# Kernel optimization log

Hardware: AMD Instinct MI355X
Metric: run time of the kernel (lower is better)

Reference implementation:

```python
import jax, jax.numpy as jnp
import numpy as np

N, E = 20000, 320000          # nodes, edges (avg in-degree ~16)
F_IN, EMB, T, OUT = 40, 40, 5, 2
F_T = EMB // T                # per-tower output width = 8
EPS_STD, EPS_GN = 1e-5, 1e-5


def _lin_init(k, fan_in, fan_out, extra=()):
    return jax.random.normal(k, (*extra, fan_in, fan_out), jnp.float32) / np.sqrt(fan_in)


def setup_inputs() -> dict:
    key = jax.random.key(0)
    ks = jax.random.split(key, 8)
    # deg histogram in init: all 20000 nodes with degree 16 -> avg_deg['log'] = log(16+1)
    return dict(
        x=jax.random.normal(ks[0], (N, F_IN), jnp.float32),
        edge_index=jax.random.randint(ks[1], (2, E), 0, N),
        W_pre=_lin_init(ks[2], 2 * F_IN, F_IN, (T,)),   # per-tower pre-MLP
        b_pre=jnp.zeros((T, F_IN), jnp.float32),
        W_post=_lin_init(ks[3], 13 * F_IN, F_T, (T,)),  # (4 agg * 3 scalers + 1 residual) * F_in
        b_post=jnp.zeros((T, F_T), jnp.float32),
        W_lin=_lin_init(ks[4], T * F_T, EMB),           # PNAConv final mixing linear
        b_lin=jnp.zeros((EMB,), jnp.float32),
        gn_weight=jnp.ones((EMB,), jnp.float32),
        gn_bias=jnp.zeros((EMB,), jnp.float32),
        gn_mean_scale=jnp.ones((EMB,), jnp.float32),
        W1=_lin_init(ks[5], EMB, EMB),                  # head hidden linear
        b1=jnp.zeros((EMB,), jnp.float32),
        W2=_lin_init(ks[6], EMB, OUT),                  # head output linear
        b2=jnp.zeros((OUT,), jnp.float32),
        avg_deg_log=jnp.float32(np.log(17.0)),
    )


def _pna_conv(x, src, dst, W_pre, b_pre, W_post, b_post, W_lin, b_lin, avg_deg_log):
    xi, xj = x[dst], x[src]                              # gather: [E, F]
    h = jnp.concatenate([xi, xj], axis=-1)               # [E, 2F]
    m = jnp.einsum('ef,tfg->etg', h, W_pre) + b_pre      # per-tower messages [E, T, F]
    cnt = jax.ops.segment_sum(jnp.ones((E,), m.dtype), dst, num_segments=N)  # in-degree [N]
    denom = jnp.maximum(cnt, 1.0)[:, None, None]
    mean = jax.ops.segment_sum(m, dst, num_segments=N) / denom
    mean2 = jax.ops.segment_sum(m * m, dst, num_segments=N) / denom
    std = jnp.sqrt(jax.nn.relu(mean2 - mean * mean) + EPS_STD)
    has = (cnt > 0)[:, None, None]
    mn = jnp.where(has, jax.ops.segment_min(m, dst, num_segments=N), 0.0)
    mx = jnp.where(has, jax.ops.segment_max(m, dst, num_segments=N), 0.0)
    agg = jnp.concatenate([mean, mn, mx, std], axis=-1)  # [N, T, 4F]
    deg = jnp.maximum(cnt, 1.0)[:, None, None]
    logd = jnp.log(deg + 1.0)
    out = jnp.concatenate(
        [agg, agg * (logd / avg_deg_log), agg * (avg_deg_log / logd)], axis=-1)  # [N, T, 12F]
    out = jnp.concatenate(
        [jnp.broadcast_to(x[:, None, :], (N, T, x.shape[-1])), out], axis=-1)    # [N, T, 13F]
    out = jnp.einsum('ntf,tfg->ntg', out, W_post) + b_post                       # [N, T, F_T]
    return out.reshape(N, T * F_T) @ W_lin + b_lin


def _graph_norm(x, w, b, mean_scale):
    mean = jnp.mean(x, axis=0, keepdims=True)
    out = x - mean_scale * mean
    var = jnp.mean(out * out, axis=0, keepdims=True)
    return w * out / jnp.sqrt(var + EPS_GN) + b


def reference(x, edge_index, W_pre, b_pre, W_post, b_post, W_lin, b_lin,
              gn_weight, gn_bias, gn_mean_scale, W1, b1, W2, b2, avg_deg_log):
    src, dst = edge_index[0], edge_index[1]
    h = _pna_conv(x, src, dst, W_pre, b_pre, W_post, b_post, W_lin, b_lin, avg_deg_log)
    h = jax.nn.relu(_graph_norm(h, gn_weight, gn_bias, gn_mean_scale))
    h = jax.nn.relu(h @ W1 + b1)   # dropout_rate=None -> no dropout
    return h @ W2 + b2
```

## Files before the change

kernel.cpp:

```cpp
#include <hip/hip_runtime.h>
#include <math.h>

#define N_NODES 20000
#define N_EDGES 320000
#define F_IN 40
#define T_TOW 5
#define EMB 40
#define NPB_PRE 16
#define NBLK_MIX 313
#define NBLK_PM 313
#define ECHUNK 16
#define STRIDE 64

typedef __attribute__((ext_vector_type(8))) _Float16 half8;
typedef __attribute__((ext_vector_type(2))) _Float16 half2_t;
typedef __attribute__((ext_vector_type(4))) float f32x4;

#define WS_STATS   0
#define WS_CURSOR  320
#define WS_SSRC    80384
#define WS_MS      5200384
#define WS_MD      13200384
#define WS_AGG     21200384
#define WS_XPOST   53200384
#define WS_H0T     69200384
#define WS_PART    72400384

__global__ __launch_bounds__(256) void k_pre(const float* __restrict__ x,
                                             const float* __restrict__ W_pre,
                                             const float* __restrict__ b_pre,
                                             const float* __restrict__ W_post,
                                             const float* __restrict__ b_post,
                                             _Float16* __restrict__ mS,
                                             _Float16* __restrict__ mD,
                                             float* __restrict__ xpostT,
                                             int* __restrict__ cursor) {
  const int tid = threadIdx.x;
  const int n0 = blockIdx.x * NPB_PRE;
  if (tid < NPB_PRE) cursor[n0 + tid] = (n0 + tid) * STRIDE;
  const bool statlane = tid < 200;
  const int q = tid - 200;
  const bool xplane = (q >= 0 && q < 40);
  const int tc = statlane ? tid : 199;
  const int t = tc / 40, g = tc - t * 40;
  const int t2 = xplane ? q / 8 : 0, g2 = xplane ? q - (q / 8) * 8 : 0;
  float wA[40], wB[40];
  const float* Wt = W_pre + t * 3200;
#pragma unroll
  for (int j = 0; j < 40; ++j) {
    wA[j] = statlane ? Wt[j * 40 + g] : W_post[t2 * 4160 + j * 8 + g2];
    wB[j] = statlane ? Wt[(40 + j) * 40 + g] : 0.f;
  }
  const float bias = statlane ? b_pre[t * 40 + g] : b_post[t2 * 8 + g2];
  for (int ni = 0; ni < NPB_PRE; ++ni) {
    const int n = n0 + ni;
    const float* xr = x + n * F_IN;
    float aA = bias, aB = 0.f;
#pragma unroll
    for (int j = 0; j < 40; j += 4) {
      const float4 xv = *(const float4*)(xr + j);
      aA += xv.x * wA[j] + xv.y * wA[j + 1] + xv.z * wA[j + 2] + xv.w * wA[j + 3];
      aB += xv.x * wB[j] + xv.y * wB[j + 1] + xv.z * wB[j + 2] + xv.w * wB[j + 3];
    }
    if (statlane) {
      mD[n * 200 + tc] = (_Float16)aA;
      mS[n * 200 + tc] = (_Float16)aB;
    } else if (xplane) {
      xpostT[t2 * (N_NODES * 8) + n * 8 + g2] = aA;
    }
  }
}

__global__ __launch_bounds__(256) void k_scatter(const int* __restrict__ src,
                                                 const int* __restrict__ dst,
                                                 int* __restrict__ cursor,
                                                 int* __restrict__ ssrc) {
  int i = blockIdx.x * 256 + threadIdx.x;
  if (i < N_EDGES) {
    int d = dst[i];
    int pos = atomicAdd(&cursor[d], 1);
    ssrc[pos] = src[i];
  }
}

__global__ __launch_bounds__(256) void k_edge(const _Float16* __restrict__ mS,
                                              const _Float16* __restrict__ mD,
                                              const int* __restrict__ cursor,
                                              const int* __restrict__ ssrc,
                                              _Float16* __restrict__ aggS) {
  const int lane = threadIdx.x & 63;
  const int wv = threadIdx.x >> 6;
  const int n = blockIdx.x * 4 + wv;
  const int r0 = n * STRIDE;
  const int r1 = __builtin_amdgcn_readfirstlane(cursor[n]);
  const int cnt = r1 - r0;
  const int cpa = lane;
  const bool bact = lane < 36;
  const int cpb = bact ? 64 + lane : 99;
  const half2_t mda = ((const half2_t*)(mD + n * 200))[cpa];
  const half2_t mdb = ((const half2_t*)(mD + n * 200))[cpb];

  const _Float16 HINF = (_Float16)65504.f;
  half2_t suma = {0, 0}, ssqa = {0, 0}, sumb = {0, 0}, ssqb = {0, 0};
  half2_t mna = {HINF, HINF}, mxa = {-HINF, -HINF};
  half2_t mnb = {HINF, HINF}, mxb = {-HINF, -HINF};
  half2_t va = {0, 0}, vb = {0, 0};

  if (cnt > 0) {
    for (int p = r0; p < r1; p += ECHUNK) {
      half2_t ha[ECHUNK], hb[ECHUNK];
#pragma unroll
      for (int i = 0; i < ECHUNK; ++i) {
        const int qe = (p + i < r1) ? (p + i) : (r1 - 1);
        const int s = __builtin_amdgcn_readfirstlane(ssrc[qe]);
        const half2_t* row = (const half2_t*)(mS + s * 200);
        ha[i] = row[cpa];
        hb[i] = row[cpb];
      }
#pragma unroll
      for (int i = 0; i < ECHUNK; ++i) {
        suma += ha[i];
        ssqa += ha[i] * ha[i];
        mna = __builtin_elementwise_min(mna, ha[i]);
        mxa = __builtin_elementwise_max(mxa, ha[i]);
        sumb += hb[i];
        ssqb += hb[i] * hb[i];
        mnb = __builtin_elementwise_min(mnb, hb[i]);
        mxb = __builtin_elementwise_max(mxb, hb[i]);
      }
      va = ha[ECHUNK - 1];
      vb = hb[ECHUNK - 1];
    }
  }

  const int padded = ((cnt + ECHUNK - 1) / ECHUNK) * ECHUNK;
  const float d = (float)(padded - cnt);
  const float inv = (cnt > 0) ? 1.f / (float)cnt : 0.f;
#pragma unroll
  for (int set = 0; set < 2; ++set) {
    if (set == 1 && !bact) break;
    const int cp = set == 0 ? cpa : cpb;
    const half2_t sum2 = set == 0 ? suma : sumb;
    const half2_t ssq2 = set == 0 ? ssqa : ssqb;
    const half2_t mn2 = set == 0 ? mna : mnb;
    const half2_t mx2 = set == 0 ? mxa : mxb;
    const half2_t vl2 = set == 0 ? va : vb;
    const half2_t md2 = set == 0 ? mda : mdb;
    half2_t omean, omn, omx, osd;
#pragma unroll
    for (int j = 0; j < 2; ++j) {
      float mean, mnf, mxf, sd;
      if (cnt > 0) {
        const float vl = (float)vl2[j];
        const float sf = (float)sum2[j] - d * vl;
        const float qf = (float)ssq2[j] - d * vl * vl;
        const float msm = sf * inv;
        const float var = qf * inv - msm * msm;
        sd = sqrtf(fmaxf(var, 0.f) + 1e-5f);
        const float mdf = (float)md2[j];
        mean = mdf + msm;
        mnf = mdf + (float)mn2[j];
        mxf = mdf + (float)mx2[j];
      } else {
        mean = 0.f; mnf = 0.f; mxf = 0.f; sd = sqrtf(1e-5f);
      }
      omean[j] = (_Float16)mean;
      omn[j] = (_Float16)mnf;
      omx[j] = (_Float16)mxf;
      osd[j] = (_Float16)sd;
    }
    const int t = cp / 20, g = 2 * (cp - t * 20);
    _Float16* abase = aggS + ((size_t)t * N_NODES + n) * 160 + g;
    *(half2_t*)(abase) = omean;
    *(half2_t*)(abase + 40) = omn;
    *(half2_t*)(abase + 80) = omx;
    *(half2_t*)(abase + 120) = osd;
  }
}

__global__ __launch_bounds__(320) void k_postmix(const _Float16* __restrict__ aggT,
                                                 const int* __restrict__ cursor,
                                                 const float* __restrict__ W_post,
                                                 const float* __restrict__ avg_dl,
                                                 const float* __restrict__ xpostT,
                                                 const float* __restrict__ W_lin,
                                                 const float* __restrict__ b_lin,
                                                 float* __restrict__ h0T,
                                                 float* __restrict__ partial) {
  __shared__ float sP[64 * 41];
  const int tid = threadIdx.x;
  const int t = tid >> 6;
  const int l = tid & 63;
  const int n0 = blockIdx.x * 64;
  const int c = l & 15;
  const int kg = l >> 4;

  const float* Wt = W_post + t * 4160;
  half8 b1f[5], b2f[5];
#pragma unroll
  for (int ks = 0; ks < 5; ++ks) {
#pragma unroll
    for (int j = 0; j < 8; ++j) {
      const int k = ks * 32 + kg * 8 + j;
      const float w1v = (c < 8) ? Wt[(40 + k) * 8 + c] : Wt[(200 + k) * 8 + (c - 8)];
      const float w2v = (c < 8) ? Wt[(360 + k) * 8 + c] : 0.f;
      b1f[ks][j] = (_Float16)w1v;
      b2f[ks][j] = (_Float16)w2v;
    }
  }
  const float avg = avg_dl[0];

  for (int tile = 0; tile < 4; ++tile) {
    const int nb = n0 + tile * 16;
    int nA = nb + c;
    if (nA >= N_NODES) nA = N_NODES - 1;
    const half8* ar = (const half8*)(aggT + ((size_t)t * N_NODES + nA) * 160);
    half8 af[5];
#pragma unroll
    for (int ks = 0; ks < 5; ++ks) af[ks] = ar[ks * 4 + kg];
    f32x4 acc1 = {0.f, 0.f, 0.f, 0.f}, acc2 = {0.f, 0.f, 0.f, 0.f};
#pragma unroll
    for (int ks = 0; ks < 5; ++ks) {
      acc1 = __builtin_amdgcn_mfma_f32_16x16x32_f16(af[ks], b1f[ks], acc1, 0, 0, 0);
      acc2 = __builtin_amdgcn_mfma_f32_16x16x32_f16(af[ks], b2f[ks], acc2, 0, 0, 0);
    }
    float bp[4];
#pragma unroll
    for (int r = 0; r < 4; ++r) bp[r] = __shfl_xor(acc1[r], 8, 64);
    if (c < 8) {
#pragma unroll
      for (int r = 0; r < 4; ++r) {
        const int nn0 = nb + kg * 4 + r;
        const int nn = (nn0 < N_NODES) ? nn0 : N_NODES - 1;
        const int cnt = cursor[nn] - nn * STRIDE;
        const float ld = logf(fmaxf((float)cnt, 1.f) + 1.f);
        const float s1 = ld / avg, s2 = avg / ld;
        const float xp = xpostT[t * (N_NODES * 8) + nn * 8 + c];
        sP[(tile * 16 + kg * 4 + r) * 41 + t * 8 + c] =
            acc1[r] + s1 * bp[r] + s2 * acc2[r] + xp;
      }
    }
  }
  __syncthreads();

  const int c0 = t * 8;
  float acc[8];
#pragma unroll
  for (int j = 0; j < 8; ++j) acc[j] = b_lin[c0 + j];
  for (int k = 0; k < 40; ++k) {
    const float p = sP[l * 41 + k];
    const float* w = W_lin + k * EMB + c0;
#pragma unroll
    for (int j = 0; j < 8; ++j) acc[j] = fmaf(p, w[j], acc[j]);
  }
  const int n = n0 + l;
  const bool ok = n < N_NODES;
  if (ok) {
#pragma unroll
    for (int j = 0; j < 8; ++j) h0T[(c0 + j) * N_NODES + n] = acc[j];
  }
#pragma unroll
  for (int j = 0; j < 8; ++j) {
    float sv = ok ? acc[j] : 0.f;
    float qv = sv * sv;
#pragma unroll
    for (int m = 32; m >= 1; m >>= 1) {
      sv += __shfl_xor(sv, m, 64);
      qv += __shfl_xor(qv, m, 64);
    }
    if (l == 0) {
      partial[blockIdx.x * 80 + c0 + j] = sv;
      partial[blockIdx.x * 80 + 40 + c0 + j] = qv;
    }
  }
}

__global__ __launch_bounds__(256) void k_stats(const float* __restrict__ partial,
                                               float* __restrict__ S1,
                                               float* __restrict__ S2) {
  const int col = blockIdx.x;
  const int tid = threadIdx.x;
  __shared__ float red[4];
  float s = 0.f;
  for (int b = tid; b < NBLK_PM; b += 256) s += partial[b * 80 + col];
#pragma unroll
  for (int m = 32; m >= 1; m >>= 1) s += __shfl_xor(s, m, 64);
  if ((tid & 63) == 0) red[tid >> 6] = s;
  __syncthreads();
  if (tid == 0) {
    const float tot = (red[0] + red[1]) + (red[2] + red[3]);
    if (col < 40) S1[col] = tot;
    else S2[col - 40] = tot;
  }
}

__global__ __launch_bounds__(256) void k_head(const float* __restrict__ S1,
                                              const float* __restrict__ S2,
                                              const float* __restrict__ h0T,
                                              const float* __restrict__ gn_w,
                                              const float* __restrict__ gn_b,
                                              const float* __restrict__ gn_ms,
                                              const float* __restrict__ W1,
                                              const float* __restrict__ b1,
                                              const float* __restrict__ W2,
                                              const float* __restrict__ b2,
                                              float* __restrict__ out) {
  __shared__ float sV[64 * 41];
  __shared__ float sH[64 * 41];
  const int tid = threadIdx.x;
  const int n0 = blockIdx.x * 64;
  const float invN = 1.f / (float)N_NODES;
  for (int i = 0; i < 10; ++i) {
    const int idx = tid + i * 256;
    const int e = idx >> 6, r = idx & 63;
    const int nn0 = n0 + r;
    const int nn = (nn0 < N_NODES) ? nn0 : 0;
    const float M = S1[e] * invN;
    const float ms = gn_ms[e];
    const float var = S2[e] * invN - ms * (2.f - ms) * M * M;
    const float sc = gn_w[e] / sqrtf(var + 1e-5f);
    const float he = h0T[e * N_NODES + nn];
    sV[r * 41 + e] = fmaxf((he - ms * M) * sc + gn_b[e], 0.f);
  }
  __syncthreads();
  const int wv = tid >> 6, lane = tid & 63;
  const int c0 = wv * 10;
  float acc[10];
#pragma unroll
  for (int j = 0; j < 10; ++j) acc[j] = b1[c0 + j];
  for (int k = 0; k < 40; ++k) {
    const float p = sV[lane * 41 + k];
    const float* w = W1 + k * EMB + c0;
#pragma unroll
    for (int j = 0; j < 10; ++j) acc[j] = fmaf(p, w[j], acc[j]);
  }
#pragma unroll
  for (int j = 0; j < 10; ++j) sH[lane * 41 + c0 + j] = fmaxf(acc[j], 0.f);
  __syncthreads();
  if (tid < 64) {
    const int n = n0 + tid;
    if (n < N_NODES) {
      float o0 = b2[0], o1 = b2[1];
      const float* hr = sH + tid * 41;
#pragma unroll
      for (int k = 0; k < 40; ++k) {
        const float r = hr[k];
        o0 = fmaf(r, W2[k * 2], o0);
        o1 = fmaf(r, W2[k * 2 + 1], o1);
      }
      out[n * 2] = o0;
      out[n * 2 + 1] = o1;
    }
  }
}

extern "C" void kernel_launch(void* const* d_in, const int* in_sizes, int n_in,
                              void* d_out, int out_size, void* d_ws, size_t ws_size,
                              hipStream_t stream) {
  const float* x      = (const float*)d_in[0];
  const int*   ei     = (const int*)d_in[1];
  const float* W_pre  = (const float*)d_in[2];
  const float* b_pre  = (const float*)d_in[3];
  const float* W_post = (const float*)d_in[4];
  const float* b_post = (const float*)d_in[5];
  const float* W_lin  = (const float*)d_in[6];
  const float* b_lin  = (const float*)d_in[7];
  const float* gn_w   = (const float*)d_in[8];
  const float* gn_b   = (const float*)d_in[9];
  const float* gn_ms  = (const float*)d_in[10];
  const float* W1     = (const float*)d_in[11];
  const float* b1     = (const float*)d_in[12];
  const float* W2     = (const float*)d_in[13];
  const float* b2     = (const float*)d_in[14];
  const float* avg_dl = (const float*)d_in[15];
  float* out = (float*)d_out;

  char* ws = (char*)d_ws;
  float* S1   = (float*)(ws + WS_STATS);
  float* S2   = S1 + 40;
  int* cursor = (int*)(ws + WS_CURSOR);
  int* ssrc   = (int*)(ws + WS_SSRC);
  _Float16* mS   = (_Float16*)(ws + WS_MS);
  _Float16* mD   = (_Float16*)(ws + WS_MD);
  _Float16* aggS = (_Float16*)(ws + WS_AGG);
  float* xpostT  = (float*)(ws + WS_XPOST);
  float* h0T     = (float*)(ws + WS_H0T);
  float* part    = (float*)(ws + WS_PART);
  const int* e_src = ei;
  const int* e_dst = ei + N_EDGES;

  k_pre<<<N_NODES / NPB_PRE, 256, 0, stream>>>(x, W_pre, b_pre, W_post, b_post,
                                               mS, mD, xpostT, cursor);
  k_scatter<<<(N_EDGES + 255) / 256, 256, 0, stream>>>(e_src, e_dst, cursor, ssrc);
  k_edge<<<N_NODES / 4, 256, 0, stream>>>(mS, mD, cursor, ssrc, aggS);
  k_postmix<<<NBLK_PM, 320, 0, stream>>>(aggS, cursor, W_post, avg_dl,
                                         xpostT, W_lin, b_lin, h0T, part);
  k_stats<<<80, 256, 0, stream>>>(part, S1, S2);
  k_head<<<NBLK_MIX, 256, 0, stream>>>(S1, S2, h0T, gn_w, gn_b, gn_ms,
                                       W1, b1, W2, b2, out);
}
```

Before: 191.7 us.

## Fuse postmix, stats and head kernels via a grid-wide atomic barrier

```diff
diff --git a/kernel.cpp b/kernel.cpp
--- a/kernel.cpp
+++ b/kernel.cpp
@@ -7,7 +7,6 @@
 #define T_TOW 5
 #define EMB 40
 #define NPB_PRE 16
-#define NBLK_MIX 313
 #define NBLK_PM 313
 #define ECHUNK 16
 #define STRIDE 64
@@ -16,7 +15,7 @@
 typedef __attribute__((ext_vector_type(2))) _Float16 half2_t;
 typedef __attribute__((ext_vector_type(4))) float f32x4;
 
-#define WS_STATS   0
+#define WS_BAR     0
 #define WS_CURSOR  320
 #define WS_SSRC    80384
 #define WS_MS      5200384
@@ -34,9 +33,11 @@
                                              _Float16* __restrict__ mS,
                                              _Float16* __restrict__ mD,
                                              float* __restrict__ xpostT,
-                                             int* __restrict__ cursor) {
+                                             int* __restrict__ cursor,
+                                             int* __restrict__ bar) {
   const int tid = threadIdx.x;
   const int n0 = blockIdx.x * NPB_PRE;
+  if (blockIdx.x == 0 && tid == 0) *bar = 0;
   if (tid < NPB_PRE) cursor[n0 + tid] = (n0 + tid) * STRIDE;
   const bool statlane = tid < 200;
   const int q = tid - 200;
@@ -178,7 +179,7 @@
   }
 }
 
-__global__ __launch_bounds__(320) void k_postmix(const _Float16* __restrict__ aggT,
+__global__ __launch_bounds__(320, 3) void k_back(const _Float16* __restrict__ aggT,
                                                  const int* __restrict__ cursor,
                                                  const float* __restrict__ W_post,
                                                  const float* __restrict__ avg_dl,
@@ -186,8 +187,19 @@
                                                  const float* __restrict__ W_lin,
                                                  const float* __restrict__ b_lin,
                                                  float* __restrict__ h0T,
-                                                 float* __restrict__ partial) {
-  __shared__ float sP[64 * 41];
+                                                 float* __restrict__ partial,
+                                                 int* __restrict__ bar,
+                                                 const float* __restrict__ gn_w,
+                                                 const float* __restrict__ gn_b,
+                                                 const float* __restrict__ gn_ms,
+                                                 const float* __restrict__ W1,
+                                                 const float* __restrict__ b1,
+                                                 const float* __restrict__ W2,
+                                                 const float* __restrict__ b2,
+                                                 float* __restrict__ out) {
+  __shared__ float sA[64 * 41];
+  __shared__ float sH[64 * 41];
+  __shared__ float sSp[4][80];
   const int tid = threadIdx.x;
   const int t = tid >> 6;
   const int l = tid & 63;
@@ -236,106 +248,103 @@
         const float ld = logf(fmaxf((float)cnt, 1.f) + 1.f);
         const float s1 = ld / avg, s2 = avg / ld;
         const float xp = xpostT[t * (N_NODES * 8) + nn * 8 + c];
-        sP[(tile * 16 + kg * 4 + r) * 41 + t * 8 + c] =
+        sA[(tile * 16 + kg * 4 + r) * 41 + t * 8 + c] =
             acc1[r] + s1 * bp[r] + s2 * acc2[r] + xp;
       }
     }
   }
   __syncthreads();
 
-  const int c0 = t * 8;
-  float acc[8];
-#pragma unroll
-  for (int j = 0; j < 8; ++j) acc[j] = b_lin[c0 + j];
-  for (int k = 0; k < 40; ++k) {
-    const float p = sP[l * 41 + k];
-    const float* w = W_lin + k * EMB + c0;
-#pragma unroll
-    for (int j = 0; j < 8; ++j) acc[j] = fmaf(p, w[j], acc[j]);
-  }
-  const int n = n0 + l;
-  const bool ok = n < N_NODES;
-  if (ok) {
-#pragma unroll
-    for (int j = 0; j < 8; ++j) h0T[(c0 + j) * N_NODES + n] = acc[j];
-  }
-#pragma unroll
-  for (int j = 0; j < 8; ++j) {
-    float sv = ok ? acc[j] : 0.f;
-    float qv = sv * sv;
-#pragma unroll
-    for (int m = 32; m >= 1; m >>= 1) {
-      sv += __shfl_xor(sv, m, 64);
-      qv += __shfl_xor(qv, m, 64);
-    }
-    if (l == 0) {
-      partial[blockIdx.x * 80 + c0 + j] = sv;
-      partial[blockIdx.x * 80 + 40 + c0 + j] = qv;
-    }
-  }
-}
-
-__global__ __launch_bounds__(256) void k_stats(const float* __restrict__ partial,
-                                               float* __restrict__ S1,
-                                               float* __restrict__ S2) {
-  const int col = blockIdx.x;
-  const int tid = threadIdx.x;
-  __shared__ float red[4];
-  float s = 0.f;
-  for (int b = tid; b < NBLK_PM; b += 256) s += partial[b * 80 + col];
-#pragma unroll
-  for (int m = 32; m >= 1; m >>= 1) s += __shfl_xor(s, m, 64);
-  if ((tid & 63) == 0) red[tid >> 6] = s;
+  {
+    const int c0 = t * 8;
+    float acc[8];
+#pragma unroll
+    for (int j = 0; j < 8; ++j) acc[j] = b_lin[c0 + j];
+    for (int k = 0; k < 40; ++k) {
+      const float p = sA[l * 41 + k];
+      const float* w = W_lin + k * EMB + c0;
+#pragma unroll
+      for (int j = 0; j < 8; ++j) acc[j] = fmaf(p, w[j], acc[j]);
+    }
+    const int n = n0 + l;
+    const bool ok = n < N_NODES;
+    if (ok) {
+#pragma unroll
+      for (int j = 0; j < 8; ++j) h0T[(c0 + j) * N_NODES + n] = acc[j];
+    }
+#pragma unroll
+    for (int j = 0; j < 8; ++j) {
+      float sv = ok ? acc[j] : 0.f;
+      float qv = sv * sv;
+#pragma unroll
+      for (int m = 32; m >= 1; m >>= 1) {
+        sv += __shfl_xor(sv, m, 64);
+        qv += __shfl_xor(qv, m, 64);
+      }
+      if (l == 0) {
+        partial[blockIdx.x * 80 + c0 + j] = sv;
+        partial[blockIdx.x * 80 + 40 + c0 + j] = qv;
+      }
+    }
+  }
+
   __syncthreads();
   if (tid == 0) {
-    const float tot = (red[0] + red[1]) + (red[2] + red[3]);
-    if (col < 40) S1[col] = tot;
-    else S2[col - 40] = tot;
-  }
-}
-
-__global__ __launch_bounds__(256) void k_head(const float* __restrict__ S1,
-                                              const float* __restrict__ S2,
-                                              const float* __restrict__ h0T,
-                                              const float* __restrict__ gn_w,
-                                              const float* __restrict__ gn_b,
-                                              const float* __restrict__ gn_ms,
-                                              const float* __restrict__ W1,
-                                              const float* __restrict__ b1,
-                                              const float* __restrict__ W2,
-                                              const float* __restrict__ b2,
-                                              float* __restrict__ out) {
-  __shared__ float sV[64 * 41];
-  __shared__ float sH[64 * 41];
-  const int tid = threadIdx.x;
-  const int n0 = blockIdx.x * 64;
+    __threadfence();
+    atomicAdd(bar, 1);
+    while (__hip_atomic_load(bar, __ATOMIC_ACQUIRE, __HIP_MEMORY_SCOPE_AGENT)
+           < NBLK_PM) {
+      __builtin_amdgcn_s_sleep(8);
+    }
+  }
+  __syncthreads();
+
+  {
+    const int part_i = tid / 80;
+    const int col = tid - part_i * 80;
+    float a0 = 0.f, a1 = 0.f, a2 = 0.f, a3 = 0.f;
+    int b = part_i;
+    for (; b + 12 < NBLK_PM; b += 16) {
+      a0 += partial[b * 80 + col];
+      a1 += partial[(b + 4) * 80 + col];
+      a2 += partial[(b + 8) * 80 + col];
+      a3 += partial[(b + 12) * 80 + col];
+    }
+    for (; b < NBLK_PM; b += 4) a0 += partial[b * 80 + col];
+    sSp[part_i][col] = (a0 + a1) + (a2 + a3);
+  }
+  __syncthreads();
+
   const float invN = 1.f / (float)N_NODES;
-  for (int i = 0; i < 10; ++i) {
-    const int idx = tid + i * 256;
+  for (int i = 0; i < 8; ++i) {
+    const int idx = tid + i * 320;
     const int e = idx >> 6, r = idx & 63;
     const int nn0 = n0 + r;
     const int nn = (nn0 < N_NODES) ? nn0 : 0;
-    const float M = S1[e] * invN;
+    const float S1e = sSp[0][e] + sSp[1][e] + sSp[2][e] + sSp[3][e];
+    const float S2e = sSp[0][40 + e] + sSp[1][40 + e] + sSp[2][40 + e] + sSp[3][40 + e];
+    const float M = S1e * invN;
     const float ms = gn_ms[e];
-    const float var = S2[e] * invN - ms * (2.f - ms) * M * M;
+    const float var = S2e * invN - ms * (2.f - ms) * M * M;
     const float sc = gn_w[e] / sqrtf(var + 1e-5f);
     const float he = h0T[e * N_NODES + nn];
-    sV[r * 41 + e] = fmaxf((he - ms * M) * sc + gn_b[e], 0.f);
-  }
-  __syncthreads();
-  const int wv = tid >> 6, lane = tid & 63;
-  const int c0 = wv * 10;
-  float acc[10];
-#pragma unroll
-  for (int j = 0; j < 10; ++j) acc[j] = b1[c0 + j];
-  for (int k = 0; k < 40; ++k) {
-    const float p = sV[lane * 41 + k];
-    const float* w = W1 + k * EMB + c0;
-#pragma unroll
-    for (int j = 0; j < 10; ++j) acc[j] = fmaf(p, w[j], acc[j]);
-  }
-#pragma unroll
-  for (int j = 0; j < 10; ++j) sH[lane * 41 + c0 + j] = fmaxf(acc[j], 0.f);
+    sA[r * 41 + e] = fmaxf((he - ms * M) * sc + gn_b[e], 0.f);
+  }
+  __syncthreads();
+  {
+    const int c0 = t * 8;
+    float acc[8];
+#pragma unroll
+    for (int j = 0; j < 8; ++j) acc[j] = b1[c0 + j];
+    for (int k = 0; k < 40; ++k) {
+      const float p = sA[l * 41 + k];
+      const float* w = W1 + k * EMB + c0;
+#pragma unroll
+      for (int j = 0; j < 8; ++j) acc[j] = fmaf(p, w[j], acc[j]);
+    }
+#pragma unroll
+    for (int j = 0; j < 8; ++j) sH[l * 41 + c0 + j] = fmaxf(acc[j], 0.f);
+  }
   __syncthreads();
   if (tid < 64) {
     const int n = n0 + tid;
@@ -376,8 +385,7 @@
   float* out = (float*)d_out;
 
   char* ws = (char*)d_ws;
-  float* S1   = (float*)(ws + WS_STATS);
-  float* S2   = S1 + 40;
+  int* bar    = (int*)(ws + WS_BAR);
   int* cursor = (int*)(ws + WS_CURSOR);
   int* ssrc   = (int*)(ws + WS_SSRC);
   _Float16* mS   = (_Float16*)(ws + WS_MS);
@@ -390,12 +398,10 @@
   const int* e_dst = ei + N_EDGES;
 
   k_pre<<<N_NODES / NPB_PRE, 256, 0, stream>>>(x, W_pre, b_pre, W_post, b_post,
-                                               mS, mD, xpostT, cursor);
+                                               mS, mD, xpostT, cursor, bar);
   k_scatter<<<(N_EDGES + 255) / 256, 256, 0, stream>>>(e_src, e_dst, cursor, ssrc);
   k_edge<<<N_NODES / 4, 256, 0, stream>>>(mS, mD, cursor, ssrc, aggS);
-  k_postmix<<<NBLK_PM, 320, 0, stream>>>(aggS, cursor, W_post, avg_dl,
-                                         xpostT, W_lin, b_lin, h0T, part);
-  k_stats<<<80, 256, 0, stream>>>(part, S1, S2);
-  k_head<<<NBLK_MIX, 256, 0, stream>>>(S1, S2, h0T, gn_w, gn_b, gn_ms,
-                                       W1, b1, W2, b2, out);
+  k_back<<<NBLK_PM, 320, 0, stream>>>(aggS, cursor, W_post, avg_dl, xpostT,
+                                      W_lin, b_lin, h0T, part, bar,
+                                      gn_w, gn_b, gn_ms, W1, b1, W2, b2, out);
 }
```

Measured after the change: 225.7 us. 17.7% more time.

## Split source messages into two half-tables and parallelize edge aggregation over halves

Applied to the files above, without the earlier changes.

```diff
diff --git a/kernel.cpp b/kernel.cpp
--- a/kernel.cpp
+++ b/kernel.cpp
@@ -7,7 +7,6 @@
 #define T_TOW 5
 #define EMB 40
 #define NPB_PRE 16
-#define NBLK_MIX 313
 #define NBLK_PM 313
 #define ECHUNK 16
 #define STRIDE 64
@@ -19,7 +18,8 @@
 #define WS_STATS   0
 #define WS_CURSOR  320
 #define WS_SSRC    80384
-#define WS_MS      5200384
+#define WS_MSA     5200384
+#define WS_MSB     9200384
 #define WS_MD      13200384
 #define WS_AGG     21200384
 #define WS_XPOST   53200384
@@ -31,7 +31,8 @@
                                              const float* __restrict__ b_pre,
                                              const float* __restrict__ W_post,
                                              const float* __restrict__ b_post,
-                                             _Float16* __restrict__ mS,
+                                             _Float16* __restrict__ mSA,
+                                             _Float16* __restrict__ mSB,
                                              _Float16* __restrict__ mD,
                                              float* __restrict__ xpostT,
                                              int* __restrict__ cursor) {
@@ -64,7 +65,8 @@
     }
     if (statlane) {
       mD[n * 200 + tc] = (_Float16)aA;
-      mS[n * 200 + tc] = (_Float16)aB;
+      if (tc < 100) mSA[n * 100 + tc] = (_Float16)aB;
+      else          mSB[n * 100 + (tc - 100)] = (_Float16)aB;
     } else if (xplane) {
       xpostT[t2 * (N_NODES * 8) + n * 8 + g2] = aA;
     }
@@ -83,7 +85,8 @@
   }
 }
 
-__global__ __launch_bounds__(256) void k_edge(const _Float16* __restrict__ mS,
+__global__ __launch_bounds__(256) void k_edge(const _Float16* __restrict__ mSA,
+                                              const _Float16* __restrict__ mSB,
                                               const _Float16* __restrict__ mD,
                                               const int* __restrict__ cursor,
                                               const int* __restrict__ ssrc,
@@ -91,90 +94,76 @@
   const int lane = threadIdx.x & 63;
   const int wv = threadIdx.x >> 6;
   const int n = blockIdx.x * 4 + wv;
+  const int p = blockIdx.y;
+  const _Float16* mSp = p ? mSB : mSA;
   const int r0 = n * STRIDE;
   const int r1 = __builtin_amdgcn_readfirstlane(cursor[n]);
   const int cnt = r1 - r0;
-  const int cpa = lane;
-  const bool bact = lane < 36;
-  const int cpb = bact ? 64 + lane : 99;
-  const half2_t mda = ((const half2_t*)(mD + n * 200))[cpa];
-  const half2_t mdb = ((const half2_t*)(mD + n * 200))[cpb];
+  const bool act = lane < 50;
+  const int cp = act ? lane : 49;
+  const int cg = p * 50 + cp;
+  const half2_t md2 = ((const half2_t*)(mD + n * 200))[cg];
 
   const _Float16 HINF = (_Float16)65504.f;
-  half2_t suma = {0, 0}, ssqa = {0, 0}, sumb = {0, 0}, ssqb = {0, 0};
-  half2_t mna = {HINF, HINF}, mxa = {-HINF, -HINF};
-  half2_t mnb = {HINF, HINF}, mxb = {-HINF, -HINF};
-  half2_t va = {0, 0}, vb = {0, 0};
+  half2_t sum2 = {0, 0}, ssq2 = {0, 0};
+  half2_t mn2 = {HINF, HINF}, mx2 = {-HINF, -HINF};
+  half2_t vl2 = {0, 0};
 
   if (cnt > 0) {
-    for (int p = r0; p < r1; p += ECHUNK) {
-      half2_t ha[ECHUNK], hb[ECHUNK];
+    for (int q = r0; q < r1; q += ECHUNK) {
+      half2_t h[ECHUNK];
 #pragma unroll
       for (int i = 0; i < ECHUNK; ++i) {
-        const int qe = (p + i < r1) ? (p + i) : (r1 - 1);
-        const int s = __builtin_amdgcn_readfirstlane(ssrc[qe]);
-        const half2_t* row = (const half2_t*)(mS + s * 200);
-        ha[i] = row[cpa];
-        hb[i] = row[cpb];
+        const int qe = (q + i < r1) ? (q + i) : (r1 - 1);
+        const int s = __builtin_amdgcn_readfirstlane(
+            __builtin_nontemporal_load(ssrc + qe));
+        h[i] = ((const half2_t*)(mSp + s * 100))[cp];
       }
 #pragma unroll
       for (int i = 0; i < ECHUNK; ++i) {
-        suma += ha[i];
-        ssqa += ha[i] * ha[i];
-        mna = __builtin_elementwise_min(mna, ha[i]);
-        mxa = __builtin_elementwise_max(mxa, ha[i]);
-        sumb += hb[i];
-        ssqb += hb[i] * hb[i];
-        mnb = __builtin_elementwise_min(mnb, hb[i]);
-        mxb = __builtin_elementwise_max(mxb, hb[i]);
+        sum2 += h[i];
+        ssq2 += h[i] * h[i];
+        mn2 = __builtin_elementwise_min(mn2, h[i]);
+        mx2 = __builtin_elementwise_max(mx2, h[i]);
       }
-      va = ha[ECHUNK - 1];
-      vb = hb[ECHUNK - 1];
+      vl2 = h[ECHUNK - 1];
     }
   }
 
   const int padded = ((cnt + ECHUNK - 1) / ECHUNK) * ECHUNK;
   const float d = (float)(padded - cnt);
   const float inv = (cnt > 0) ? 1.f / (float)cnt : 0.f;
-#pragma unroll
-  for (int set = 0; set < 2; ++set) {
-    if (set == 1 && !bact) break;
-    const int cp = set == 0 ? cpa : cpb;
-    const half2_t sum2 = set == 0 ? suma : sumb;
-    const half2_t ssq2 = set == 0 ? ssqa : ssqb;
-    const half2_t mn2 = set == 0 ? mna : mnb;
-    const half2_t mx2 = set == 0 ? mxa : mxb;
-    const half2_t vl2 = set == 0 ? va : vb;
-    const half2_t md2 = set == 0 ? mda : mdb;
-    half2_t omean, omn, omx, osd;
-#pragma unroll
-    for (int j = 0; j < 2; ++j) {
-      float mean, mnf, mxf, sd;
-      if (cnt > 0) {
-        const float vl = (float)vl2[j];
-        const float sf = (float)sum2[j] - d * vl;
-        const float qf = (float)ssq2[j] - d * vl * vl;
-        const float msm = sf * inv;
-        const float var = qf * inv - msm * msm;
-        sd = sqrtf(fmaxf(var, 0.f) + 1e-5f);
-        const float mdf = (float)md2[j];
-        mean = mdf + msm;
-        mnf = mdf + (float)mn2[j];
-        mxf = mdf + (float)mx2[j];
-      } else {
-        mean = 0.f; mnf = 0.f; mxf = 0.f; sd = sqrtf(1e-5f);
-      }
-      omean[j] = (_Float16)mean;
-      omn[j] = (_Float16)mnf;
-      omx[j] = (_Float16)mxf;
-      osd[j] = (_Float16)sd;
-    }
-    const int t = cp / 20, g = 2 * (cp - t * 20);
+  half2_t omean, omn, omx, osd;
+#pragma unroll
+  for (int j = 0; j < 2; ++j) {
+    float mean, mnf, mxf, sd;
+    if (cnt > 0) {
+      const float vl = (float)vl2[j];
+      const float sf = (float)sum2[j] - d * vl;
+      const float qf = (float)ssq2[j] - d * vl * vl;
+      const float msm = sf * inv;
+      const float var = qf * inv - msm * msm;
+      sd = sqrtf(fmaxf(var, 0.f) + 1e-5f);
+      const float mdf = (float)md2[j];
+      mean = mdf + msm;
+      mnf = mdf + (float)mn2[j];
+      mxf = mdf + (float)mx2[j];
+    } else {
+      mean = 0.f; mnf = 0.f; mxf = 0.f; sd = sqrtf(1e-5f);
+    }
+    omean[j] = (_Float16)mean;
+    omn[j] = (_Float16)mnf;
+    omx[j] = (_Float16)mxf;
+    osd[j] = (_Float16)sd;
+  }
+  if (act) {
+    const int c0 = 2 * cg;
+    const int t = c0 / 40, g = c0 - t * 40;
     _Float16* abase = aggS + ((size_t)t * N_NODES + n) * 160 + g;
-    *(half2_t*)(abase) = omean;
-    *(half2_t*)(abase + 40) = omn;
-    *(half2_t*)(abase + 80) = omx;
-    *(half2_t*)(abase + 120) = osd;
+    __builtin_nontemporal_store(omean, (half2_t*)(abase));
+    __builtin_nontemporal_store(omn,   (half2_t*)(abase + 40));
+    __builtin_nontemporal_store(omx,   (half2_t*)(abase + 80));
+    __builtin_nontemporal_store(osd,   (half2_t*)(abase + 120));
   }
 }
 
@@ -380,7 +369,8 @@
   float* S2   = S1 + 40;
   int* cursor = (int*)(ws + WS_CURSOR);
   int* ssrc   = (int*)(ws + WS_SSRC);
-  _Float16* mS   = (_Float16*)(ws + WS_MS);
+  _Float16* mSA  = (_Float16*)(ws + WS_MSA);
+  _Float16* mSB  = (_Float16*)(ws + WS_MSB);
   _Float16* mD   = (_Float16*)(ws + WS_MD);
   _Float16* aggS = (_Float16*)(ws + WS_AGG);
   float* xpostT  = (float*)(ws + WS_XPOST);
@@ -390,12 +380,12 @@
   const int* e_dst = ei + N_EDGES;
 
   k_pre<<<N_NODES / NPB_PRE, 256, 0, stream>>>(x, W_pre, b_pre, W_post, b_post,
-                                               mS, mD, xpostT, cursor);
+                                               mSA, mSB, mD, xpostT, cursor);
   k_scatter<<<(N_EDGES + 255) / 256, 256, 0, stream>>>(e_src, e_dst, cursor, ssrc);
-  k_edge<<<N_NODES / 4, 256, 0, stream>>>(mS, mD, cursor, ssrc, aggS);
+  k_edge<<<dim3(N_NODES / 4, 2), 256, 0, stream>>>(mSA, mSB, mD, cursor, ssrc, aggS);
   k_postmix<<<NBLK_PM, 320, 0, stream>>>(aggS, cursor, W_post, avg_dl,
                                          xpostT, W_lin, b_lin, h0T, part);
   k_stats<<<80, 256, 0, stream>>>(part, S1, S2);
-  k_head<<<NBLK_MIX, 256, 0, stream>>>(S1, S2, h0T, gn_w, gn_b, gn_ms,
-                                       W1, b1, W2, b2, out);
-}
+  k_head<<<NBLK_PM, 256, 0, stream>>>(S1, S2, h0T, gn_w, gn_b, gn_ms,
+                                      W1, b1, W2, b2, out);
+}
```

Result: slower. 207.1 us (+8.0%).
